# Kernel optimization log

Measured on AMD Instinct MI355X. Metric: run time of the kernel, lower is better.

Reference implementation:

```python
import jax, jax.numpy as jnp
import numpy as np

B, C, W, H, Z = 2, 32, 96, 96, 64
IC = C  # inter_channels defaults to in_channels (required by depthwise g conv)
THRESH = 1.5
EPS = 1e-5


def setup_inputs() -> dict:
    key = jax.random.key(0)
    ks = jax.random.split(key, 12)
    s1 = 1.0 / np.sqrt(C)   # 1x1x1 conv fan-in
    s3 = 1.0 / np.sqrt(3.0) # depthwise (1,1,3) conv fan-in per channel
    return {
        "x": jax.random.normal(ks[0], (B, C, W, H, Z), jnp.float32),
        # per-sample spacings in [0,3): mixes both branches around thresh 1.5
        "spacings": jax.random.uniform(ks[1], (B, 3), jnp.float32) * 3.0,
        "theta_w": jax.random.normal(ks[2], (IC, C), jnp.float32) * s1,
        "theta_b": jax.random.normal(ks[3], (IC,), jnp.float32) * s1,
        "phi_w": jax.random.normal(ks[4], (IC, C), jnp.float32) * s1,
        "phi_b": jax.random.normal(ks[5], (IC,), jnp.float32) * s1,
        "g_w": jax.random.normal(ks[6], (C, 3), jnp.float32) * s3,   # depthwise kernel along z
        "g_b": jax.random.normal(ks[7], (C,), jnp.float32) * s3,
        "W_w": jax.random.normal(ks[8], (C, IC), jnp.float32) * s1,
        "W_b": jax.random.normal(ks[9], (C,), jnp.float32) * s1,
        # torch inits BN gamma=0, beta=0 (zero-init residual trick); use small random
        "bn_gamma": jax.random.normal(ks[10], (C,), jnp.float32) * 0.1,
        "bn_beta": jax.random.normal(ks[11], (C,), jnp.float32) * 0.1,
    }


def _cvec(v):
    return v.reshape(1, -1, 1, 1, 1)


def _conv1x1(h, w, b):
    # 1x1x1 Conv3d == channel-mixing matmul
    return jnp.einsum('bcwhz,oc->bowhz', h, w) + _cvec(b)


def reference(x, spacings, theta_w, theta_b, phi_w, phi_b, g_w, g_b, W_w, W_b, bn_gamma, bn_beta):
    # theta/phi: 1x1x1 convs -> (B, IC, W, H, Z)
    t = _conv1x1(x, theta_w, theta_b)
    p = _conv1x1(x, phi_w, phi_b)

    # g: depthwise conv along z, kernel 3, pad 1 (groups=C)
    xp = jnp.pad(x, ((0, 0), (0, 0), (0, 0), (0, 0), (1, 1)))
    gx = (xp[..., :-2] * _cvec(g_w[:, 0])
          + xp[..., 1:-1] * _cvec(g_w[:, 1])
          + xp[..., 2:] * _cvec(g_w[:, 2])
          + _cvec(g_b))

    # non-local attention along z per (b, w, h) row: scores (B, W, H, Z, Z)
    f = jnp.einsum('bcwhz,bcwhy->bwhzy', t, p)
    a = jax.nn.softmax(f, axis=-1)
    y = jnp.einsum('bwhzy,bcwhy->bcwhz', a, gx)
    nl = y + x  # residual inside compute_x

    # per-sample branch on z-spacing, vectorized with where
    mask = (spacings[:, -1] <= THRESH).reshape(-1, 1, 1, 1, 1)
    res = jnp.where(mask, nl, x)

    # W: 1x1x1 conv + BatchNorm3d (training-mode batch stats)
    out = _conv1x1(res, W_w, W_b)
    mean = jnp.mean(out, axis=(0, 2, 3, 4), keepdims=True)
    var = jnp.var(out, axis=(0, 2, 3, 4), keepdims=True)
    out = (out - mean) * jax.lax.rsqrt(var + EPS)
    return out * _cvec(bn_gamma) + _cvec(bn_beta)
```

## Files before the change

### kernel.cpp

```cpp
#include <hip/hip_runtime.h>
#include <stdint.h>

#define CHS 589824
#define ROWS 18432
#define WHn 9216
#define NRED 1179648.0f
#define LOG2E 1.4426950408889634f

typedef short s16x8 __attribute__((ext_vector_type(8)));
typedef float f32x4v __attribute__((ext_vector_type(4)));

#define MFMA16 __builtin_amdgcn_mfma_f32_16x16x32_bf16

#define WSFRAG 10240

#define OXH 0
#define OP  8704
#define OG  13312
#define LDSZ 17664

static __device__ __forceinline__ uint16_t bfh(float v) {
    union { __bf16 h; uint16_t u; } c; c.h = (__bf16)v; return c.u;
}
static __device__ __forceinline__ float bf2f(uint16_t u) {
    union { uint32_t x; float f; } c; c.x = (uint32_t)u << 16; return c.f;
}
static __device__ __forceinline__ uint32_t pk2u(uint16_t a, uint16_t b) {
    return (uint32_t)a | ((uint32_t)b << 16);
}
static __device__ __forceinline__ uint32_t pkbf(float a, float b) {
    return pk2u(bfh(a), bfh(b));
}
static __device__ __forceinline__ float ex2(float x) {
    float r;
    asm("v_exp_f32 %0, %1" : "=v"(r) : "v"(x));
    return r;
}
static __device__ __forceinline__ s16x8 rd8(const char* p) {
    union { uint64_t q[2]; s16x8 s; } v;
    v.q[0] = *(const uint64_t*)p;
    v.q[1] = *(const uint64_t*)(p + 8);
    return v.s;
}

static __device__ __forceinline__ void wfrag2(const float* __restrict__ Wp, int mt, int l15, int kb,
                                              float sc, s16x8& hi, s16x8& lo) {
    const float* p = Wp + (l15 + 16*mt)*32 + 8*kb;
    const float4 f0 = *(const float4*)p;
    const float4 f1 = *(const float4*)(p + 4);
    float f[8] = {f0.x*sc, f0.y*sc, f0.z*sc, f0.w*sc, f1.x*sc, f1.y*sc, f1.z*sc, f1.w*sc};
    union { uint32_t u[4]; s16x8 v; } rh, rl;
    #pragma unroll
    for (int i = 0; i < 4; ++i) {
        const uint16_t h0 = bfh(f[2*i]), h1 = bfh(f[2*i+1]);
        rh.u[i] = pk2u(h0, h1);
        rl.u[i] = pk2u(bfh(f[2*i] - bf2f(h0)), bfh(f[2*i+1] - bf2f(h1)));
    }
    hi = rh.v; lo = rl.v;
}
static __device__ __forceinline__ s16x8 wfragW(const float* __restrict__ Wp, int mt, int l15, int kb) {
    const float* p = Wp + (l15 + 16*mt)*32;
    const float4 f0 = *(const float4*)(p + 4*kb);
    const float4 f1 = *(const float4*)(p + 16 + 4*kb);
    union { uint32_t u[4]; s16x8 v; } r;
    r.u[0] = pkbf(f0.x, f0.y); r.u[1] = pkbf(f0.z, f0.w);
    r.u[2] = pkbf(f1.x, f1.y); r.u[3] = pkbf(f1.z, f1.w);
    return r.v;
}

__global__ __launch_bounds__(256) void k0_frag(
    const float* __restrict__ theta_w, const float* __restrict__ phi_w,
    const float* __restrict__ Ww, char* __restrict__ ws)
{
    const int tid = threadIdx.x;
    const int m = tid >> 7;
    const int r = tid & 127;
    const int mt = r >> 6, l = r & 63;
    s16x8 hi, lo;
    wfrag2(m ? phi_w : theta_w, mt, l & 15, l >> 4, m ? 1.0f : LOG2E, hi, lo);
    *(s16x8*)(ws + m*4096 + (mt*64 + l)*16)        = hi;
    *(s16x8*)(ws + m*4096 + 2048 + (mt*64 + l)*16) = lo;
    if (tid < 128) {
        const int mtw = tid >> 6, lw = tid & 63;
        *(s16x8*)(ws + 8192 + (mtw*64 + lw)*16) = wfragW(Ww, mtw, lw & 15, lw >> 4);
    }
}

__global__ __launch_bounds__(256, 8) void k1_row(
    const float* __restrict__ x, const float* __restrict__ spacings,
    const float* __restrict__ theta_b, const float* __restrict__ phi_b,
    const float* __restrict__ g_w, const float* __restrict__ g_b,
    const float* __restrict__ Wb, const char* __restrict__ frags,
    float* __restrict__ out, float* __restrict__ part)
{
    __shared__ __align__(16) char lds[LDSZ];
    const int t = threadIdx.x;
    const int wv = t >> 6, l = t & 63;
    const int l15 = l & 15, kb = l >> 4;
    const int row = blockIdx.x;
    const int b = row / WHn, wh = row - b*WHn;
    const long base = (long)b*32*CHS + (long)wh*64;
    const int zr = 16*wv + l15;

    float xv[8];
    #pragma unroll
    for (int j = 0; j < 8; ++j) xv[j] = x[base + (long)(8*wv + j)*CHS + l];
    #pragma unroll
    for (int j = 0; j < 4; ++j) {
        const uint16_t h0 = bfh(xv[2*j]), h1 = bfh(xv[2*j+1]);
        *(uint32_t*)(lds + OXH + l*136 + (8*wv + 2*j)*2)      = pk2u(h0, h1);
        *(uint32_t*)(lds + OXH + l*136 + 64 + (8*wv + 2*j)*2) =
            pk2u(bfh(xv[2*j] - bf2f(h0)), bfh(xv[2*j+1] - bf2f(h1)));
    }
    const int pG = 32*(l >> 5) + 8*((l >> 2) & 3) + 4*((l >> 4) & 1) + (l & 3);
    #pragma unroll
    for (int j = 0; j < 8; ++j) {
        const int c = 8*wv + j;
        float xm = __shfl_up(xv[j], 1);   if (l == 0)  xm = 0.f;
        float xp = __shfl_down(xv[j], 1); if (l == 63) xp = 0.f;
        const float g = g_w[3*c]*xm + g_w[3*c+1]*xv[j] + g_w[3*c+2]*xp + g_b[c];
        *(uint16_t*)(lds + OG + c*136 + 2*pG) = bfh(g);
    }
    __syncthreads();

    s16x8 bth, btl;
    {
        const s16x8 bxh = rd8(lds + OXH + zr*136 + 16*kb);
        const s16x8 bxl = rd8(lds + OXH + zr*136 + 64 + 16*kb);
        const s16x8 t0h = *(const s16x8*)(frags + l*16);
        const s16x8 t1h = *(const s16x8*)(frags + 1024 + l*16);
        const s16x8 t0l = *(const s16x8*)(frags + 2048 + l*16);
        const s16x8 t1l = *(const s16x8*)(frags + 3072 + l*16);
        const float4 b0 = *(const float4*)(theta_b + 4*kb);
        const float4 b1 = *(const float4*)(theta_b + 16 + 4*kb);
        f32x4v T0; T0[0]=b0.x*LOG2E; T0[1]=b0.y*LOG2E; T0[2]=b0.z*LOG2E; T0[3]=b0.w*LOG2E;
        f32x4v T1; T1[0]=b1.x*LOG2E; T1[1]=b1.y*LOG2E; T1[2]=b1.z*LOG2E; T1[3]=b1.w*LOG2E;
        T0 = MFMA16(t0h, bxh, T0, 0, 0, 0);
        T0 = MFMA16(t0h, bxl, T0, 0, 0, 0);
        T0 = MFMA16(t0l, bxh, T0, 0, 0, 0);
        T1 = MFMA16(t1h, bxh, T1, 0, 0, 0);
        T1 = MFMA16(t1h, bxl, T1, 0, 0, 0);
        T1 = MFMA16(t1l, bxh, T1, 0, 0, 0);
        const s16x8 p0h = *(const s16x8*)(frags + 4096 + l*16);
        const s16x8 p1h = *(const s16x8*)(frags + 4096 + 1024 + l*16);
        const s16x8 p0l = *(const s16x8*)(frags + 4096 + 2048 + l*16);
        const s16x8 p1l = *(const s16x8*)(frags + 4096 + 3072 + l*16);
        const float4 c0 = *(const float4*)(phi_b + 4*kb);
        const float4 c1 = *(const float4*)(phi_b + 16 + 4*kb);
        f32x4v P0; P0[0]=c0.x; P0[1]=c0.y; P0[2]=c0.z; P0[3]=c0.w;
        f32x4v P1; P1[0]=c1.x; P1[1]=c1.y; P1[2]=c1.z; P1[3]=c1.w;
        P0 = MFMA16(p0h, bxh, P0, 0, 0, 0);
        P0 = MFMA16(p0h, bxl, P0, 0, 0, 0);
        P0 = MFMA16(p0l, bxh, P0, 0, 0, 0);
        P1 = MFMA16(p1h, bxh, P1, 0, 0, 0);
        P1 = MFMA16(p1h, bxl, P1, 0, 0, 0);
        P1 = MFMA16(p1l, bxh, P1, 0, 0, 0);
        union { uint32_t u[2]; uint64_t q; } w;
        w.u[0] = pkbf(P0[0], P0[1]); w.u[1] = pkbf(P0[2], P0[3]);
        *(uint64_t*)(lds + OP + zr*72 + 16*kb) = w.q;
        w.u[0] = pkbf(P1[0], P1[1]); w.u[1] = pkbf(P1[2], P1[3]);
        *(uint64_t*)(lds + OP + zr*72 + 16*kb + 8) = w.q;
        uint16_t h[8];
        #pragma unroll
        for (int r = 0; r < 4; ++r) { h[r] = bfh(T0[r]); h[4+r] = bfh(T1[r]); }
        union { uint32_t u[4]; s16x8 s; } H, L;
        H.u[0] = pk2u(h[0], h[1]); H.u[1] = pk2u(h[2], h[3]);
        H.u[2] = pk2u(h[4], h[5]); H.u[3] = pk2u(h[6], h[7]);
        L.u[0] = pkbf(T0[0]-bf2f(h[0]), T0[1]-bf2f(h[1]));
        L.u[1] = pkbf(T0[2]-bf2f(h[2]), T0[3]-bf2f(h[3]));
        L.u[2] = pkbf(T1[0]-bf2f(h[4]), T1[1]-bf2f(h[5]));
        L.u[3] = pkbf(T1[2]-bf2f(h[6]), T1[3]-bf2f(h[7]));
        bth = H.s; btl = L.s;
    }
    __syncthreads();

    f32x4v Fq[4];
    #pragma unroll
    for (int yt = 0; yt < 4; ++yt) {
        const s16x8 pah = rd8(lds + OP + (16*yt + l15)*72 + 16*kb);
        f32x4v zz; zz[0]=0.f; zz[1]=0.f; zz[2]=0.f; zz[3]=0.f;
        zz = MFMA16(pah, bth, zz, 0, 0, 0);
        zz = MFMA16(pah, btl, zz, 0, 0, 0);
        Fq[yt] = zz;
    }

    s16x8 apk[2];
    float inv;
    {
        float mx = -3.4e38f;
        #pragma unroll
        for (int yt = 0; yt < 4; ++yt)
            #pragma unroll
            for (int r = 0; r < 4; ++r) mx = fmaxf(mx, Fq[yt][r]);
        mx = fmaxf(mx, __shfl_xor(mx, 16));
        mx = fmaxf(mx, __shfl_xor(mx, 32));
        float p[4][4]; float sum = 0.f;
        #pragma unroll
        for (int yt = 0; yt < 4; ++yt)
            #pragma unroll
            for (int r = 0; r < 4; ++r) { p[yt][r] = ex2(Fq[yt][r] - mx); sum += p[yt][r]; }
        sum += __shfl_xor(sum, 16);
        sum += __shfl_xor(sum, 32);
        inv = 1.0f / sum;
        #pragma unroll
        for (int ks = 0; ks < 2; ++ks) {
            union { uint32_t u[4]; s16x8 s; } A;
            A.u[0] = pkbf(p[2*ks][0],   p[2*ks][1]);
            A.u[1] = pkbf(p[2*ks][2],   p[2*ks][3]);
            A.u[2] = pkbf(p[2*ks+1][0], p[2*ks+1][1]);
            A.u[3] = pkbf(p[2*ks+1][2], p[2*ks+1][3]);
            apk[ks] = A.s;
        }
    }

    s16x8 brf;
    {
        f32x4v Yq[2];
        #pragma unroll
        for (int r = 0; r < 4; ++r) { Yq[0][r] = 0.f; Yq[1][r] = 0.f; }
        #pragma unroll
        for (int ks = 0; ks < 2; ++ks) {
            #pragma unroll
            for (int mt = 0; mt < 2; ++mt) {
                const s16x8 gA = rd8(lds + OG + (16*mt + l15)*136 + 64*ks + 16*kb);
                Yq[mt] = MFMA16(gA, apk[ks], Yq[mt], 0, 0, 0);
            }
        }
        const bool msk = spacings[b*3 + 2] <= 1.5f;
        union { uint32_t u[4]; s16x8 s; } R;
        #pragma unroll
        for (int mt = 0; mt < 2; ++mt) {
            const uint64_t xh = *(const uint64_t*)(lds + OXH + zr*136 + (16*mt + 4*kb)*2);
            float rv[4];
            #pragma unroll
            for (int r = 0; r < 4; ++r) {
                const float xr = bf2f((uint16_t)(xh >> (16*r)));
                rv[r] = msk ? fmaf(Yq[mt][r], inv, xr) : xr;
            }
            R.u[2*mt]   = pkbf(rv[0], rv[1]);
            R.u[2*mt+1] = pkbf(rv[2], rv[3]);
        }
        brf = R.s;
    }

    {
        f32x4v accs[2];
        #pragma unroll
        for (int mt = 0; mt < 2; ++mt) {
            const s16x8 aW = *(const s16x8*)(frags + 8192 + (mt*64 + l)*16);
            const float4 wb4 = *(const float4*)(Wb + 16*mt + 4*kb);
            f32x4v acc; acc[0]=wb4.x; acc[1]=wb4.y; acc[2]=wb4.z; acc[3]=wb4.w;
            acc = MFMA16(aW, brf, acc, 0, 0, 0);
            accs[mt] = acc;
        }
        float* op = out + base + zr;
        #pragma unroll
        for (int mt = 0; mt < 2; ++mt)
            #pragma unroll
            for (int r = 0; r < 4; ++r)
                op[(long)(16*mt + 4*kb + r)*CHS] = accs[mt][r];
        const int sr = row*4 + wv;
        float bs[8];
        #pragma unroll
        for (int mt = 0; mt < 2; ++mt)
            #pragma unroll
            for (int r = 0; r < 4; ++r) bs[4*mt+r] = accs[mt][r];
        #pragma unroll
        for (int off = 1; off < 16; off <<= 1)
            #pragma unroll
            for (int i = 0; i < 8; ++i) bs[i] += __shfl_xor(bs[i], off);
        if (l15 == 0) {
            #pragma unroll
            for (int mt = 0; mt < 2; ++mt)
                #pragma unroll
                for (int r = 0; r < 4; ++r)
                    part[sr*64 + 16*mt + 4*kb + r] = bs[4*mt+r];
        }
        #pragma unroll
        for (int mt = 0; mt < 2; ++mt)
            #pragma unroll
            for (int r = 0; r < 4; ++r) { const float v = accs[mt][r]; bs[4*mt+r] = v*v; }
        #pragma unroll
        for (int off = 1; off < 16; off <<= 1)
            #pragma unroll
            for (int i = 0; i < 8; ++i) bs[i] += __shfl_xor(bs[i], off);
        if (l15 == 0) {
            #pragma unroll
            for (int mt = 0; mt < 2; ++mt)
                #pragma unroll
                for (int r = 0; r < 4; ++r)
                    part[sr*64 + 32 + 16*mt + 4*kb + r] = bs[4*mt+r];
        }
    }
}

__global__ __launch_bounds__(256) void k2a(const float* __restrict__ part,
                                           float* __restrict__ part2)
{
    __shared__ float red[4][64];
    const int t = threadIdx.x, lane = t & 63, grp = t >> 6;
    const int p = blockIdx.x;
    float s = 0.f;
    for (int k = 0; k < 72; ++k) s += part[(p*288 + grp + 4*k)*64 + lane];
    red[grp][lane] = s;
    __syncthreads();
    if (t < 64) part2[p*64 + t] = red[0][t] + red[1][t] + red[2][t] + red[3][t];
}

__global__ __launch_bounds__(256) void k2b(const float* __restrict__ part2,
    const float* __restrict__ gamma, const float* __restrict__ beta,
    float* __restrict__ sc)
{
    __shared__ float red[4][64];
    __shared__ float tot[64];
    const int t = threadIdx.x, lane = t & 63, grp = t >> 6;
    float s = 0.f;
    for (int k = 0; k < 64; ++k) s += part2[(grp + 4*k)*64 + lane];
    red[grp][lane] = s;
    __syncthreads();
    if (t < 64) tot[t] = red[0][t] + red[1][t] + red[2][t] + red[3][t];
    __syncthreads();
    if (t < 32) {
        const float mean = tot[t] / NRED;
        const float var  = tot[32+t] / NRED - mean*mean;
        const float rstd = rsqrtf(var + 1e-5f);
        const float scale = gamma[t] * rstd;
        sc[t]    = scale;
        sc[32+t] = fmaf(-mean, scale, beta[t]);
    }
}

__global__ __launch_bounds__(256) void k3_norm(float* __restrict__ out,
                                               const float* __restrict__ sc)
{
    __shared__ float s[64];
    if (threadIdx.x < 64) s[threadIdx.x] = sc[threadIdx.x];
    __syncthreads();
    const int total4 = 2*32*CHS/4;
    const int Q = CHS/4;
    for (int i = blockIdx.x*256 + threadIdx.x; i < total4; i += gridDim.x*256) {
        float4 v = ((const float4*)out)[i];
        const int c = (i / Q) & 31;
        const float scale = s[c], shift = s[32+c];
        v.x = fmaf(v.x, scale, shift);
        v.y = fmaf(v.y, scale, shift);
        v.z = fmaf(v.z, scale, shift);
        v.w = fmaf(v.w, scale, shift);
        ((float4*)out)[i] = v;
    }
}

extern "C" void kernel_launch(void* const* d_in, const int* in_sizes, int n_in,
                              void* d_out, int out_size, void* d_ws, size_t ws_size,
                              hipStream_t stream) {
    const float* x        = (const float*)d_in[0];
    const float* spacings = (const float*)d_in[1];
    const float* theta_w  = (const float*)d_in[2];
    const float* theta_b  = (const float*)d_in[3];
    const float* phi_w    = (const float*)d_in[4];
    const float* phi_b    = (const float*)d_in[5];
    const float* g_w      = (const float*)d_in[6];
    const float* g_b      = (const float*)d_in[7];
    const float* Ww       = (const float*)d_in[8];
    const float* Wb       = (const float*)d_in[9];
    const float* gamma    = (const float*)d_in[10];
    const float* beta     = (const float*)d_in[11];
    float* out   = (float*)d_out;
    char*  frags = (char*)d_ws;
    float* part  = (float*)((char*)d_ws + WSFRAG);
    float* part2 = part + (size_t)ROWS*256;
    float* sc    = part2 + 256*64;

    hipLaunchKernelGGL(k0_frag, dim3(1), dim3(256), 0, stream, theta_w, phi_w, Ww, frags);
    hipLaunchKernelGGL(k1_row, dim3(ROWS), dim3(256), 0, stream,
                       x, spacings, theta_b, phi_b, g_w, g_b, Wb, frags, out, part);
    hipLaunchKernelGGL(k2a, dim3(256), dim3(256), 0, stream, part, part2);
    hipLaunchKernelGGL(k2b, dim3(1), dim3(256), 0, stream, part2, gamma, beta, sc);
    hipLaunchKernelGGL(k3_norm, dim3(4096), dim3(256), 0, stream, out, sc);
}
```

Measured before the change: 184.6 us.

## Process two attention rows per block in k1_row to amortize fragment loads

Each k1_row block now handles two adjacent (b,w,h) rows, with doubled LDS and half the grid. Weight fragments and biases are loaded once and reused for both rows, and the two rows' MFMA chains are interleaved, which is meant to raise instruction-level parallelism and cut per-block overhead. In exchange, the occupancy hint drops from 8 to 4 blocks, and register and LDS pressure per block roughly double.

```diff
diff --git a/kernel.cpp b/kernel.cpp
--- a/kernel.cpp
+++ b/kernel.cpp
@@ -17,7 +17,8 @@
 #define OXH 0
 #define OP  8704
 #define OG  13312
-#define LDSZ 17664
+#define ROWL 17664
+#define LDSZ (2*ROWL)
 
 static __device__ __forceinline__ uint16_t bfh(float v) {
     union { __bf16 h; uint16_t u; } c; c.h = (__bf16)v; return c.u;
@@ -86,7 +87,7 @@
     }
 }
 
-__global__ __launch_bounds__(256, 8) void k1_row(
+__global__ __launch_bounds__(256, 4) void k1_row(
     const float* __restrict__ x, const float* __restrict__ spacings,
     const float* __restrict__ theta_b, const float* __restrict__ phi_b,
     const float* __restrict__ g_w, const float* __restrict__ g_b,
@@ -97,111 +98,134 @@
     const int t = threadIdx.x;
     const int wv = t >> 6, l = t & 63;
     const int l15 = l & 15, kb = l >> 4;
-    const int row = blockIdx.x;
-    const int b = row / WHn, wh = row - b*WHn;
+    const int row0 = blockIdx.x*2;
+    const int b = row0 / WHn, wh = row0 - b*WHn;
     const long base = (long)b*32*CHS + (long)wh*64;
     const int zr = 16*wv + l15;
 
-    float xv[8];
     #pragma unroll
-    for (int j = 0; j < 8; ++j) xv[j] = x[base + (long)(8*wv + j)*CHS + l];
-    #pragma unroll
-    for (int j = 0; j < 4; ++j) {
-        const uint16_t h0 = bfh(xv[2*j]), h1 = bfh(xv[2*j+1]);
-        *(uint32_t*)(lds + OXH + l*136 + (8*wv + 2*j)*2)      = pk2u(h0, h1);
-        *(uint32_t*)(lds + OXH + l*136 + 64 + (8*wv + 2*j)*2) =
-            pk2u(bfh(xv[2*j] - bf2f(h0)), bfh(xv[2*j+1] - bf2f(h1)));
-    }
-    const int pG = 32*(l >> 5) + 8*((l >> 2) & 3) + 4*((l >> 4) & 1) + (l & 3);
-    #pragma unroll
-    for (int j = 0; j < 8; ++j) {
-        const int c = 8*wv + j;
-        float xm = __shfl_up(xv[j], 1);   if (l == 0)  xm = 0.f;
-        float xp = __shfl_down(xv[j], 1); if (l == 63) xp = 0.f;
-        const float g = g_w[3*c]*xm + g_w[3*c+1]*xv[j] + g_w[3*c+2]*xp + g_b[c];
-        *(uint16_t*)(lds + OG + c*136 + 2*pG) = bfh(g);
-    }
-    __syncthreads();
-
-    s16x8 bth, btl;
+    for (int rr = 0; rr < 2; ++rr) {
+        char* L = lds + rr*ROWL;
+        const float* xp = x + base + rr*64;
+        float xv[8];
+        #pragma unroll
+        for (int j = 0; j < 8; ++j) xv[j] = xp[(long)(8*wv + j)*CHS + l];
+        #pragma unroll
+        for (int j = 0; j < 4; ++j) {
+            const uint16_t h0 = bfh(xv[2*j]), h1 = bfh(xv[2*j+1]);
+            *(uint32_t*)(L + OXH + l*136 + (8*wv + 2*j)*2)      = pk2u(h0, h1);
+            *(uint32_t*)(L + OXH + l*136 + 64 + (8*wv + 2*j)*2) =
+                pk2u(bfh(xv[2*j] - bf2f(h0)), bfh(xv[2*j+1] - bf2f(h1)));
+        }
+        const int pG = 32*(l >> 5) + 8*((l >> 2) & 3) + 4*((l >> 4) & 1) + (l & 3);
+        #pragma unroll
+        for (int j = 0; j < 8; ++j) {
+            const int c = 8*wv + j;
+            float xm = __shfl_up(xv[j], 1);   if (l == 0)  xm = 0.f;
+            float xp2 = __shfl_down(xv[j], 1); if (l == 63) xp2 = 0.f;
+            const float g = g_w[3*c]*xm + g_w[3*c+1]*xv[j] + g_w[3*c+2]*xp2 + g_b[c];
+            *(uint16_t*)(L + OG + c*136 + 2*pG) = bfh(g);
+        }
+    }
+    __syncthreads();
+
+    s16x8 bth[2], btl[2];
     {
-        const s16x8 bxh = rd8(lds + OXH + zr*136 + 16*kb);
-        const s16x8 bxl = rd8(lds + OXH + zr*136 + 64 + 16*kb);
-        const s16x8 t0h = *(const s16x8*)(frags + l*16);
-        const s16x8 t1h = *(const s16x8*)(frags + 1024 + l*16);
-        const s16x8 t0l = *(const s16x8*)(frags + 2048 + l*16);
-        const s16x8 t1l = *(const s16x8*)(frags + 3072 + l*16);
-        const float4 b0 = *(const float4*)(theta_b + 4*kb);
-        const float4 b1 = *(const float4*)(theta_b + 16 + 4*kb);
-        f32x4v T0; T0[0]=b0.x*LOG2E; T0[1]=b0.y*LOG2E; T0[2]=b0.z*LOG2E; T0[3]=b0.w*LOG2E;
-        f32x4v T1; T1[0]=b1.x*LOG2E; T1[1]=b1.y*LOG2E; T1[2]=b1.z*LOG2E; T1[3]=b1.w*LOG2E;
-        T0 = MFMA16(t0h, bxh, T0, 0, 0, 0);
-        T0 = MFMA16(t0h, bxl, T0, 0, 0, 0);
-        T0 = MFMA16(t0l, bxh, T0, 0, 0, 0);
-        T1 = MFMA16(t1h, bxh, T1, 0, 0, 0);
-        T1 = MFMA16(t1h, bxl, T1, 0, 0, 0);
-        T1 = MFMA16(t1l, bxh, T1, 0, 0, 0);
-        const s16x8 p0h = *(const s16x8*)(frags + 4096 + l*16);
-        const s16x8 p1h = *(const s16x8*)(frags + 4096 + 1024 + l*16);
-        const s16x8 p0l = *(const s16x8*)(frags + 4096 + 2048 + l*16);
-        const s16x8 p1l = *(const s16x8*)(frags + 4096 + 3072 + l*16);
-        const float4 c0 = *(const float4*)(phi_b + 4*kb);
-        const float4 c1 = *(const float4*)(phi_b + 16 + 4*kb);
-        f32x4v P0; P0[0]=c0.x; P0[1]=c0.y; P0[2]=c0.z; P0[3]=c0.w;
-        f32x4v P1; P1[0]=c1.x; P1[1]=c1.y; P1[2]=c1.z; P1[3]=c1.w;
-        P0 = MFMA16(p0h, bxh, P0, 0, 0, 0);
-        P0 = MFMA16(p0h, bxl, P0, 0, 0, 0);
-        P0 = MFMA16(p0l, bxh, P0, 0, 0, 0);
-        P1 = MFMA16(p1h, bxh, P1, 0, 0, 0);
-        P1 = MFMA16(p1h, bxl, P1, 0, 0, 0);
-        P1 = MFMA16(p1l, bxh, P1, 0, 0, 0);
-        union { uint32_t u[2]; uint64_t q; } w;
-        w.u[0] = pkbf(P0[0], P0[1]); w.u[1] = pkbf(P0[2], P0[3]);
-        *(uint64_t*)(lds + OP + zr*72 + 16*kb) = w.q;
-        w.u[0] = pkbf(P1[0], P1[1]); w.u[1] = pkbf(P1[2], P1[3]);
-        *(uint64_t*)(lds + OP + zr*72 + 16*kb + 8) = w.q;
-        uint16_t h[8];
-        #pragma unroll
-        for (int r = 0; r < 4; ++r) { h[r] = bfh(T0[r]); h[4+r] = bfh(T1[r]); }
-        union { uint32_t u[4]; s16x8 s; } H, L;
-        H.u[0] = pk2u(h[0], h[1]); H.u[1] = pk2u(h[2], h[3]);
-        H.u[2] = pk2u(h[4], h[5]); H.u[3] = pk2u(h[6], h[7]);
-        L.u[0] = pkbf(T0[0]-bf2f(h[0]), T0[1]-bf2f(h[1]));
-        L.u[1] = pkbf(T0[2]-bf2f(h[2]), T0[3]-bf2f(h[3]));
-        L.u[2] = pkbf(T1[0]-bf2f(h[4]), T1[1]-bf2f(h[5]));
-        L.u[3] = pkbf(T1[2]-bf2f(h[6]), T1[3]-bf2f(h[7]));
-        bth = H.s; btl = L.s;
-    }
-    __syncthreads();
-
-    f32x4v Fq[4];
+        s16x8 bxh[2], bxl[2];
+        #pragma unroll
+        for (int rr = 0; rr < 2; ++rr) {
+            bxh[rr] = rd8(lds + rr*ROWL + OXH + zr*136 + 16*kb);
+            bxl[rr] = rd8(lds + rr*ROWL + OXH + zr*136 + 64 + 16*kb);
+        }
+        {
+            const s16x8 t0h = *(const s16x8*)(frags + l*16);
+            const s16x8 t1h = *(const s16x8*)(frags + 1024 + l*16);
+            const s16x8 t0l = *(const s16x8*)(frags + 2048 + l*16);
+            const s16x8 t1l = *(const s16x8*)(frags + 3072 + l*16);
+            const float4 b0 = *(const float4*)(theta_b + 4*kb);
+            const float4 b1 = *(const float4*)(theta_b + 16 + 4*kb);
+            #pragma unroll
+            for (int rr = 0; rr < 2; ++rr) {
+                f32x4v T0; T0[0]=b0.x*LOG2E; T0[1]=b0.y*LOG2E; T0[2]=b0.z*LOG2E; T0[3]=b0.w*LOG2E;
+                f32x4v T1; T1[0]=b1.x*LOG2E; T1[1]=b1.y*LOG2E; T1[2]=b1.z*LOG2E; T1[3]=b1.w*LOG2E;
+                T0 = MFMA16(t0h, bxh[rr], T0, 0, 0, 0);
+                T0 = MFMA16(t0h, bxl[rr], T0, 0, 0, 0);
+                T0 = MFMA16(t0l, bxh[rr], T0, 0, 0, 0);
+                T1 = MFMA16(t1h, bxh[rr], T1, 0, 0, 0);
+                T1 = MFMA16(t1h, bxl[rr], T1, 0, 0, 0);
+                T1 = MFMA16(t1l, bxh[rr], T1, 0, 0, 0);
+                uint16_t h[8];
+                #pragma unroll
+                for (int r = 0; r < 4; ++r) { h[r] = bfh(T0[r]); h[4+r] = bfh(T1[r]); }
+                union { uint32_t u[4]; s16x8 s; } H, L2;
+                H.u[0] = pk2u(h[0], h[1]); H.u[1] = pk2u(h[2], h[3]);
+                H.u[2] = pk2u(h[4], h[5]); H.u[3] = pk2u(h[6], h[7]);
+                L2.u[0] = pkbf(T0[0]-bf2f(h[0]), T0[1]-bf2f(h[1]));
+                L2.u[1] = pkbf(T0[2]-bf2f(h[2]), T0[3]-bf2f(h[3]));
+                L2.u[2] = pkbf(T1[0]-bf2f(h[4]), T1[1]-bf2f(h[5]));
+                L2.u[3] = pkbf(T1[2]-bf2f(h[6]), T1[3]-bf2f(h[7]));
+                bth[rr] = H.s; btl[rr] = L2.s;
+            }
+        }
+        {
+            const s16x8 p0h = *(const s16x8*)(frags + 4096 + l*16);
+            const s16x8 p1h = *(const s16x8*)(frags + 4096 + 1024 + l*16);
+            const s16x8 p0l = *(const s16x8*)(frags + 4096 + 2048 + l*16);
+            const s16x8 p1l = *(const s16x8*)(frags + 4096 + 3072 + l*16);
+            const float4 c0 = *(const float4*)(phi_b + 4*kb);
+            const float4 c1 = *(const float4*)(phi_b + 16 + 4*kb);
+            #pragma unroll
+            for (int rr = 0; rr < 2; ++rr) {
+                f32x4v P0; P0[0]=c0.x; P0[1]=c0.y; P0[2]=c0.z; P0[3]=c0.w;
+                f32x4v P1; P1[0]=c1.x; P1[1]=c1.y; P1[2]=c1.z; P1[3]=c1.w;
+                P0 = MFMA16(p0h, bxh[rr], P0, 0, 0, 0);
+                P0 = MFMA16(p0h, bxl[rr], P0, 0, 0, 0);
+                P0 = MFMA16(p0l, bxh[rr], P0, 0, 0, 0);
+                P1 = MFMA16(p1h, bxh[rr], P1, 0, 0, 0);
+                P1 = MFMA16(p1h, bxl[rr], P1, 0, 0, 0);
+                P1 = MFMA16(p1l, bxh[rr], P1, 0, 0, 0);
+                union { uint32_t u[2]; uint64_t q; } w;
+                w.u[0] = pkbf(P0[0], P0[1]); w.u[1] = pkbf(P0[2], P0[3]);
+                *(uint64_t*)(lds + rr*ROWL + OP + zr*72 + 16*kb) = w.q;
+                w.u[0] = pkbf(P1[0], P1[1]); w.u[1] = pkbf(P1[2], P1[3]);
+                *(uint64_t*)(lds + rr*ROWL + OP + zr*72 + 16*kb + 8) = w.q;
+            }
+        }
+    }
+    __syncthreads();
+
+    f32x4v Fq[2][4];
     #pragma unroll
     for (int yt = 0; yt < 4; ++yt) {
-        const s16x8 pah = rd8(lds + OP + (16*yt + l15)*72 + 16*kb);
-        f32x4v zz; zz[0]=0.f; zz[1]=0.f; zz[2]=0.f; zz[3]=0.f;
-        zz = MFMA16(pah, bth, zz, 0, 0, 0);
-        zz = MFMA16(pah, btl, zz, 0, 0, 0);
-        Fq[yt] = zz;
-    }
-
-    s16x8 apk[2];
-    float inv;
-    {
+        #pragma unroll
+        for (int rr = 0; rr < 2; ++rr) {
+            const s16x8 pah = rd8(lds + rr*ROWL + OP + (16*yt + l15)*72 + 16*kb);
+            f32x4v zz; zz[0]=0.f; zz[1]=0.f; zz[2]=0.f; zz[3]=0.f;
+            zz = MFMA16(pah, bth[rr], zz, 0, 0, 0);
+            zz = MFMA16(pah, btl[rr], zz, 0, 0, 0);
+            Fq[rr][yt] = zz;
+        }
+    }
+
+    s16x8 apk[2][2];
+    float inv[2];
+    #pragma unroll
+    for (int rr = 0; rr < 2; ++rr) {
         float mx = -3.4e38f;
         #pragma unroll
         for (int yt = 0; yt < 4; ++yt)
             #pragma unroll
-            for (int r = 0; r < 4; ++r) mx = fmaxf(mx, Fq[yt][r]);
+            for (int r = 0; r < 4; ++r) mx = fmaxf(mx, Fq[rr][yt][r]);
         mx = fmaxf(mx, __shfl_xor(mx, 16));
         mx = fmaxf(mx, __shfl_xor(mx, 32));
         float p[4][4]; float sum = 0.f;
         #pragma unroll
         for (int yt = 0; yt < 4; ++yt)
             #pragma unroll
-            for (int r = 0; r < 4; ++r) { p[yt][r] = ex2(Fq[yt][r] - mx); sum += p[yt][r]; }
+            for (int r = 0; r < 4; ++r) { p[yt][r] = ex2(Fq[rr][yt][r] - mx); sum += p[yt][r]; }
         sum += __shfl_xor(sum, 16);
         sum += __shfl_xor(sum, 32);
-        inv = 1.0f / sum;
+        inv[rr] = 1.0f / sum;
         #pragma unroll
         for (int ks = 0; ks < 2; ++ks) {
             union { uint32_t u[4]; s16x8 s; } A;
@@ -209,12 +233,14 @@
             A.u[1] = pkbf(p[2*ks][2],   p[2*ks][3]);
             A.u[2] = pkbf(p[2*ks+1][0], p[2*ks+1][1]);
             A.u[3] = pkbf(p[2*ks+1][2], p[2*ks+1][3]);
-            apk[ks] = A.s;
-        }
-    }
-
-    s16x8 brf;
-    {
+            apk[rr][ks] = A.s;
+        }
+    }
+
+    const bool msk = spacings[b*3 + 2] <= 1.5f;
+    s16x8 brf[2];
+    #pragma unroll
+    for (int rr = 0; rr < 2; ++rr) {
         f32x4v Yq[2];
         #pragma unroll
         for (int r = 0; r < 4; ++r) { Yq[0][r] = 0.f; Yq[1][r] = 0.f; }
@@ -222,74 +248,76 @@
         for (int ks = 0; ks < 2; ++ks) {
             #pragma unroll
             for (int mt = 0; mt < 2; ++mt) {
-                const s16x8 gA = rd8(lds + OG + (16*mt + l15)*136 + 64*ks + 16*kb);
-                Yq[mt] = MFMA16(gA, apk[ks], Yq[mt], 0, 0, 0);
-            }
-        }
-        const bool msk = spacings[b*3 + 2] <= 1.5f;
+                const s16x8 gA = rd8(lds + rr*ROWL + OG + (16*mt + l15)*136 + 64*ks + 16*kb);
+                Yq[mt] = MFMA16(gA, apk[rr][ks], Yq[mt], 0, 0, 0);
+            }
+        }
         union { uint32_t u[4]; s16x8 s; } R;
         #pragma unroll
         for (int mt = 0; mt < 2; ++mt) {
-            const uint64_t xh = *(const uint64_t*)(lds + OXH + zr*136 + (16*mt + 4*kb)*2);
+            const uint64_t xh = *(const uint64_t*)(lds + rr*ROWL + OXH + zr*136 + (16*mt + 4*kb)*2);
             float rv[4];
             #pragma unroll
             for (int r = 0; r < 4; ++r) {
                 const float xr = bf2f((uint16_t)(xh >> (16*r)));
-                rv[r] = msk ? fmaf(Yq[mt][r], inv, xr) : xr;
+                rv[r] = msk ? fmaf(Yq[mt][r], inv[rr], xr) : xr;
             }
             R.u[2*mt]   = pkbf(rv[0], rv[1]);
             R.u[2*mt+1] = pkbf(rv[2], rv[3]);
         }
-        brf = R.s;
+        brf[rr] = R.s;
     }
 
     {
-        f32x4v accs[2];
-        #pragma unroll
-        for (int mt = 0; mt < 2; ++mt) {
-            const s16x8 aW = *(const s16x8*)(frags + 8192 + (mt*64 + l)*16);
-            const float4 wb4 = *(const float4*)(Wb + 16*mt + 4*kb);
-            f32x4v acc; acc[0]=wb4.x; acc[1]=wb4.y; acc[2]=wb4.z; acc[3]=wb4.w;
-            acc = MFMA16(aW, brf, acc, 0, 0, 0);
-            accs[mt] = acc;
-        }
-        float* op = out + base + zr;
-        #pragma unroll
-        for (int mt = 0; mt < 2; ++mt)
-            #pragma unroll
-            for (int r = 0; r < 4; ++r)
-                op[(long)(16*mt + 4*kb + r)*CHS] = accs[mt][r];
-        const int sr = row*4 + wv;
-        float bs[8];
-        #pragma unroll
-        for (int mt = 0; mt < 2; ++mt)
-            #pragma unroll
-            for (int r = 0; r < 4; ++r) bs[4*mt+r] = accs[mt][r];
-        #pragma unroll
-        for (int off = 1; off < 16; off <<= 1)
-            #pragma unroll
-            for (int i = 0; i < 8; ++i) bs[i] += __shfl_xor(bs[i], off);
-        if (l15 == 0) {
+        const s16x8 aW0 = *(const s16x8*)(frags + 8192 + l*16);
+        const s16x8 aW1 = *(const s16x8*)(frags + 8192 + (64 + l)*16);
+        const float4 wb0 = *(const float4*)(Wb + 4*kb);
+        const float4 wb1 = *(const float4*)(Wb + 16 + 4*kb);
+        #pragma unroll
+        for (int rr = 0; rr < 2; ++rr) {
+            f32x4v accs[2];
+            f32x4v a0; a0[0]=wb0.x; a0[1]=wb0.y; a0[2]=wb0.z; a0[3]=wb0.w;
+            f32x4v a1; a1[0]=wb1.x; a1[1]=wb1.y; a1[2]=wb1.z; a1[3]=wb1.w;
+            accs[0] = MFMA16(aW0, brf[rr], a0, 0, 0, 0);
+            accs[1] = MFMA16(aW1, brf[rr], a1, 0, 0, 0);
+            float* op = out + base + rr*64 + zr;
             #pragma unroll
             for (int mt = 0; mt < 2; ++mt)
                 #pragma unroll
                 for (int r = 0; r < 4; ++r)
-                    part[sr*64 + 16*mt + 4*kb + r] = bs[4*mt+r];
-        }
-        #pragma unroll
-        for (int mt = 0; mt < 2; ++mt)
-            #pragma unroll
-            for (int r = 0; r < 4; ++r) { const float v = accs[mt][r]; bs[4*mt+r] = v*v; }
-        #pragma unroll
-        for (int off = 1; off < 16; off <<= 1)
-            #pragma unroll
-            for (int i = 0; i < 8; ++i) bs[i] += __shfl_xor(bs[i], off);
-        if (l15 == 0) {
+                    op[(long)(16*mt + 4*kb + r)*CHS] = accs[mt][r];
+            const int sr = (row0 + rr)*4 + wv;
+            float bs[8];
             #pragma unroll
             for (int mt = 0; mt < 2; ++mt)
                 #pragma unroll
-                for (int r = 0; r < 4; ++r)
-                    part[sr*64 + 32 + 16*mt + 4*kb + r] = bs[4*mt+r];
+                for (int r = 0; r < 4; ++r) bs[4*mt+r] = accs[mt][r];
+            #pragma unroll
+            for (int off = 1; off < 16; off <<= 1)
+                #pragma unroll
+                for (int i = 0; i < 8; ++i) bs[i] += __shfl_xor(bs[i], off);
+            if (l15 == 0) {
+                #pragma unroll
+                for (int mt = 0; mt < 2; ++mt)
+                    #pragma unroll
+                    for (int r = 0; r < 4; ++r)
+                        part[sr*64 + 16*mt + 4*kb + r] = bs[4*mt+r];
+            }
+            #pragma unroll
+            for (int mt = 0; mt < 2; ++mt)
+                #pragma unroll
+                for (int r = 0; r < 4; ++r) { const float v = accs[mt][r]; bs[4*mt+r] = v*v; }
+            #pragma unroll
+            for (int off = 1; off < 16; off <<= 1)
+                #pragma unroll
+                for (int i = 0; i < 8; ++i) bs[i] += __shfl_xor(bs[i], off);
+            if (l15 == 0) {
+                #pragma unroll
+                for (int mt = 0; mt < 2; ++mt)
+                    #pragma unroll
+                    for (int r = 0; r < 4; ++r)
+                        part[sr*64 + 32 + 16*mt + 4*kb + r] = bs[4*mt+r];
+            }
         }
     }
 }
@@ -372,7 +400,7 @@
     float* sc    = part2 + 256*64;
 
     hipLaunchKernelGGL(k0_frag, dim3(1), dim3(256), 0, stream, theta_w, phi_w, Ww, frags);
-    hipLaunchKernelGGL(k1_row, dim3(ROWS), dim3(256), 0, stream,
+    hipLaunchKernelGGL(k1_row, dim3(ROWS/2), dim3(256), 0, stream,
                        x, spacings, theta_b, phi_b, g_w, g_b, Wb, frags, out, part);
     hipLaunchKernelGGL(k2a, dim3(256), dim3(256), 0, stream, part, part2);
     hipLaunchKernelGGL(k2b, dim3(1), dim3(256), 0, stream, part2, gamma, beta, sc);
```

Measured after the change: 178.4 us. 3.4% less time.
